# Performance work log

Measured on AMD Instinct MI355X. Metric: run time of the kernel, lower is better.

Reference implementation:

```python
import jax, jax.numpy as jnp
import numpy as np

B, T, IN, H, OUT = 1024, 512, 16, 64, 8


def setup_inputs() -> dict:
    key = jax.random.key(0)
    ks = jax.random.split(key, 7)
    s = 1.0 / np.sqrt(H)
    return {
        "x": jax.random.normal(ks[0], (B, T, IN), dtype=jnp.float32),
        "W_ih": jax.random.normal(ks[1], (4 * H, IN), dtype=jnp.float32) * s,
        "W_hh": jax.random.normal(ks[2], (4 * H, H), dtype=jnp.float32) * s,
        "b_ih": jax.random.normal(ks[3], (4 * H,), dtype=jnp.float32) * s,
        "b_hh": jax.random.normal(ks[4], (4 * H,), dtype=jnp.float32) * s,
        "W_fc": jax.random.normal(ks[5], (OUT, H), dtype=jnp.float32) * s,
        "b_fc": jax.random.normal(ks[6], (OUT,), dtype=jnp.float32) * s,
    }


def reference(x, W_ih, W_hh, b_ih, b_hh, W_fc, b_fc):
    Bq, Tq, _ = x.shape
    Hq = W_hh.shape[1]
    # Precompute input contribution for all timesteps: [T, B, 4H]
    xw = jnp.einsum("bti,gi->tbg", x, W_ih) + b_ih + b_hh

    def step(carry, xw_t):
        h, c = carry
        gates = xw_t + h @ W_hh.T  # [B, 4H]
        i, f, g, o = jnp.split(gates, 4, axis=-1)  # PyTorch gate order i,f,g,o
        i = jax.nn.sigmoid(i)
        f = jax.nn.sigmoid(f)
        g = jnp.tanh(g)
        o = jax.nn.sigmoid(o)
        c = f * c + i * g
        h = o * jnp.tanh(c)
        return (h, c), None

    h0 = jnp.zeros((Bq, Hq), dtype=x.dtype)
    c0 = jnp.zeros((Bq, Hq), dtype=x.dtype)
    (h_last, _), _ = jax.lax.scan(step, (h0, c0), xw)

    # fc on last timestep only, then sigmoid -> [B, 1, OUT]
    out = jax.nn.sigmoid(h_last @ W_fc.T + b_fc)
    return out[:, None, :]
```

## Files before the change

### kernel.cpp

```cpp
#include <hip/hip_runtime.h>
#include <math.h>


#define LSTM_T 512
#define LSTM_IN 16
#define LSTM_H 64
#define LSTM_OUT 8
#define BT 2
#define HSTRIDE 136

#define L2E   1.44269504088896340736f
#define L2E2  2.88539008177792681472f

typedef _Float16 half8  __attribute__((ext_vector_type(8)));
typedef float    floatx4 __attribute__((ext_vector_type(4)));

static __device__ __forceinline__ float fast_rcp(float x) { return __builtin_amdgcn_rcpf(x); }
static __device__ __forceinline__ float fast_exp2(float x) { return __builtin_amdgcn_exp2f(x); }
static __device__ __forceinline__ float sigm2(float p) { return fast_rcp(1.0f + fast_exp2(-p)); }
static __device__ __forceinline__ void pin4(int4& v) {
    asm volatile("" : "+v"(v.x), "+v"(v.y), "+v"(v.z), "+v"(v.w));
}
static __device__ __forceinline__ void pinf4(float4& v) {
    asm volatile("" : "+v"(v.x), "+v"(v.y), "+v"(v.z), "+v"(v.w));
}
static __device__ __forceinline__ void lite_barrier() {
    asm volatile("s_waitcnt lgkmcnt(0)\n\ts_barrier" ::: "memory");
}
static __device__ __forceinline__ unsigned pk2h(float a, float b) {
    return __builtin_bit_cast(unsigned, __builtin_amdgcn_cvt_pkrtz(a, b));
}
static __device__ __forceinline__ half8 to_h8(float4 a, float4 b) {
    uint4 u = make_uint4(pk2h(a.x, a.y), pk2h(a.z, a.w), pk2h(b.x, b.y), pk2h(b.z, b.w));
    return __builtin_bit_cast(half8, u);
}
static __device__ __forceinline__ int4 cvt8h(float4 a, float4 b) {
    return __builtin_bit_cast(int4, to_h8(a, b));
}
static __device__ __forceinline__ float4 ld4(const float* p) {
    return *reinterpret_cast<const float4*>(p);
}
static __device__ __forceinline__ float4 scl4(float4 v, float s) {
    return make_float4(s * v.x, s * v.y, s * v.z, s * v.w);
}
static __device__ __forceinline__ float sel4(floatx4 v, bool r0, bool r1) {
    float lo = r0 ? v[1] : v[0];
    float hi = r0 ? v[3] : v[2];
    return r1 ? hi : lo;
}
static __device__ __forceinline__ float dpp8(float v) {
    int r = __builtin_amdgcn_update_dpp(0, __builtin_bit_cast(int, v),
                                        0x128, 0xF, 0xF, false);
    return __builtin_bit_cast(float, r);
}

__global__ __launch_bounds__(256, 2)
void lstm_mfma_kernel(const float* __restrict__ x,
                      const float* __restrict__ W_ih,
                      const float* __restrict__ W_hh,
                      const float* __restrict__ b_ih,
                      const float* __restrict__ b_hh,
                      const float* __restrict__ W_fc,
                      const float* __restrict__ b_fc,
                      float* __restrict__ out) {
    const int tid   = threadIdx.x;
    const int lane  = tid & 63;
    const int w     = tid >> 6;
    const int q     = lane >> 4;
    const int m     = lane & 15;
    const int b     = m & 1;
    const int rho   = (m >> 1) & 3;
    const bool r0   = (rho & 1) != 0;
    const bool r1   = (rho & 2) != 0;
    const bool h1   = (m & 8) != 0;
    const int jmine = 16 * w + 4 * q + rho;
    const bool wr   = (m < 8);
    const int woff  = b * HSTRIDE + jmine + (h1 ? 64 : 0);
    const int bbase = blockIdx.x * BT;

    const float a1 = h1 ? 1.0f : 0.0f;
    const float b1 = h1 ? -2.0f : 1.0f;

    __shared__ __align__(16) _Float16 hbuf[2][BT][HSTRIDE];
    __shared__ __align__(16) float hfin[BT][LSTM_H];

    int4 Ah[4][2], Ax[4];
    float4 bias4[4];
    #pragma unroll
    for (int tt = 0; tt < 4; ++tt) {
        const float sc = (tt == 2) ? L2E2 : -L2E;
        const int gt = tt * 64 + 16 * w + m;
        #pragma unroll
        for (int c = 0; c < 2; ++c) {
            const float* s = W_hh + gt * LSTM_H + 32 * c + 8 * q;
            Ah[tt][c] = cvt8h(scl4(ld4(s), sc), scl4(ld4(s + 4), sc));
            pin4(Ah[tt][c]);
        }
        float4 xa = make_float4(0.f, 0.f, 0.f, 0.f), xb = xa;
        if (q < 2) {
            const float* s = W_ih + gt * LSTM_IN + 8 * q;
            xa = ld4(s); xb = ld4(s + 4);
        }
        Ax[tt] = cvt8h(scl4(xa, sc), scl4(xb, sc));
        pin4(Ax[tt]);
        const int gb = tt * 64 + 16 * w + 4 * q;
        float4 bi = ld4(b_ih + gb), bh = ld4(b_hh + gb);
        bias4[tt] = make_float4(sc * (bi.x + bh.x), sc * (bi.y + bh.y),
                                sc * (bi.z + bh.z), sc * (bi.w + bh.w));
        pinf4(bias4[tt]);
    }

    if (tid < 64) {
        int bb = tid >> 5, jj = tid & 31;
        reinterpret_cast<int*>(&hbuf[0][bb][0])[jj] = 0;
    }

    const float* xp = x + (size_t)(bbase + b) * LSTM_T * LSTM_IN + 8 * q;
    float4 xA0 = make_float4(0.f, 0.f, 0.f, 0.f), xA1 = xA0;
    float4 xB0 = xA0, xB1 = xA0;
    if (q < 2) {
        xA0 = ld4(xp);              xA1 = ld4(xp + 4);
        xB0 = ld4(xp + LSTM_IN);    xB1 = ld4(xp + LSTM_IN + 4);
    }
    __syncthreads();

    float cs = 0.0f, hreg = 0.0f;

#define STEP(T_, X0, X1)                                                        \
    {                                                                           \
        const _Float16* cur = &hbuf[(T_) & 1][0][0];                            \
        _Float16*       nxt = &hbuf[((T_) + 1) & 1][0][0];                      \
         \
        half8 bh0 = *reinterpret_cast<const half8*>(cur + b * HSTRIDE + 8 * q); \
        half8 bh1 = *reinterpret_cast<const half8*>(cur + b * HSTRIDE + 32 + 8 * q); \
        half8 xf = to_h8(X0, X1);                                               \
        floatx4 acc[4];                                                         \
        _Pragma("unroll")                                                       \
        for (int tt = 0; tt < 4; ++tt)                                          \
            acc[tt] = __builtin_amdgcn_mfma_f32_16x16x32_f16(                   \
                __builtin_bit_cast(half8, Ax[tt]), xf,                          \
                __builtin_bit_cast(floatx4, bias4[tt]), 0, 0, 0);               \
                       \
        if (q < 2 && (T_) + 2 < LSTM_T) {                                       \
            X0 = ld4(xp + (size_t)((T_) + 2) * LSTM_IN);                        \
            X1 = ld4(xp + (size_t)((T_) + 2) * LSTM_IN + 4);                    \
        }                                                                       \
        _Pragma("unroll")                                                       \
        for (int tt = 0; tt < 4; ++tt)                                          \
            acc[tt] = __builtin_amdgcn_mfma_f32_16x16x32_f16(                   \
                __builtin_bit_cast(half8, Ah[tt][0]), bh0, acc[tt], 0, 0, 0);   \
        _Pragma("unroll")                                                       \
        for (int tt = 0; tt < 4; ++tt)                                          \
            acc[tt] = __builtin_amdgcn_mfma_f32_16x16x32_f16(                   \
                __builtin_bit_cast(half8, Ah[tt][1]), bh1, acc[tt], 0, 0, 0);   \
        __builtin_amdgcn_s_setprio(1);                                          \
               \
        floatx4 v1, v2;                                                         \
        _Pragma("unroll")                                                       \
        for (int r = 0; r < 4; ++r) {                                           \
            v1[r] = h1 ? acc[2][r] : acc[1][r];                                 \
            v2[r] = h1 ? acc[3][r] : acc[0][r];                                 \
        }                                                                       \
        float u1 = sel4(v1, r0, r1);                                            \
        float u2 = sel4(v2, r0, r1);                                            \
                  \
        float act1 = fmaf(b1, fast_rcp(1.0f + fast_exp2(u1)), a1);              \
        float act2 = fast_rcp(1.0f + fast_exp2(u2));          \
        float act2K = act2 * L2E2;                   \
            \
        float g_in = dpp8(act1);                                                \
        float o_in = dpp8(act2);                                                \
        \
        cs = fmaf(act1, cs, act2K * g_in);                                      \
        float th = fmaf(-2.0f, fast_rcp(1.0f + fast_exp2(cs)), 1.0f);           \
        hreg = o_in * th;                                                       \
                   \
        nxt[woff] = (_Float16)hreg;                                             \
        __builtin_amdgcn_s_setprio(0);                                          \
        lite_barrier();                                                         \
    }

    for (int t = 0; t < LSTM_T; t += 2) {
        STEP(t,     xA0, xA1)
        STEP(t + 1, xB0, xB1)
    }
#undef STEP

    if (wr) hfin[b][jmine] = hreg;
    __syncthreads();

    if (tid < BT * LSTM_OUT) {
        int bb = tid >> 3, o = tid & 7;
        float s = b_fc[o];
        #pragma unroll
        for (int j4 = 0; j4 < LSTM_H / 4; ++j4) {
            float4 wv = ld4(W_fc + o * LSTM_H + 4 * j4);
            float4 hv = *reinterpret_cast<const float4*>(&hfin[bb][4 * j4]);
            s = fmaf(wv.x, hv.x, s);
            s = fmaf(wv.y, hv.y, s);
            s = fmaf(wv.z, hv.z, s);
            s = fmaf(wv.w, hv.w, s);
        }
        out[(size_t)(bbase + bb) * LSTM_OUT + o] = sigm2(s * L2E);
    }
}

extern "C" void kernel_launch(void* const* d_in, const int* in_sizes, int n_in,
                              void* d_out, int out_size, void* d_ws, size_t ws_size,
                              hipStream_t stream) {
    const float* x    = (const float*)d_in[0];
    const float* W_ih = (const float*)d_in[1];
    const float* W_hh = (const float*)d_in[2];
    const float* b_ih = (const float*)d_in[3];
    const float* b_hh = (const float*)d_in[4];
    const float* W_fc = (const float*)d_in[5];
    const float* b_fc = (const float*)d_in[6];
    float* out = (float*)d_out;

    lstm_mfma_kernel<<<1024 / BT, 256, 0, stream>>>(
        x, W_ih, W_hh, b_ih, b_hh, W_fc, b_fc, out);
}
```

Before: 251.4 us.

## Process four batch rows per block and pipeline input MFMAs off the critical path

Each block now handles four batch rows instead of two, with every lane computing all four gates for its own (batch, hidden) element. This drops the split-gate layout and the DPP exchange. The input-projection MFMA for the next step is issued after the recurrent MFMAs, so only the two h-dependent MFMAs sit on the serial dependency chain. Occupancy is lowered to one block per SIMD set and the grid is halved, which trades fewer blocks and less latency hiding for fewer barriers per row and more useful lanes per MFMA.

```diff
diff --git a/kernel.cpp b/kernel.cpp
--- a/kernel.cpp
+++ b/kernel.cpp
@@ -6,8 +6,8 @@
 #define LSTM_IN 16
 #define LSTM_H 64
 #define LSTM_OUT 8
-#define BT 2
-#define HSTRIDE 136
+#define BT 4
+#define HSTRIDE 80
 
 #define L2E   1.44269504088896340736f
 #define L2E2  2.88539008177792681472f
@@ -48,13 +48,8 @@
     float hi = r0 ? v[3] : v[2];
     return r1 ? hi : lo;
 }
-static __device__ __forceinline__ float dpp8(float v) {
-    int r = __builtin_amdgcn_update_dpp(0, __builtin_bit_cast(int, v),
-                                        0x128, 0xF, 0xF, false);
-    return __builtin_bit_cast(float, r);
-}
-
-__global__ __launch_bounds__(256, 2)
+
+__global__ __launch_bounds__(256, 1)
 void lstm_mfma_kernel(const float* __restrict__ x,
                       const float* __restrict__ W_ih,
                       const float* __restrict__ W_hh,
@@ -68,21 +63,15 @@
     const int w     = tid >> 6;
     const int q     = lane >> 4;
     const int m     = lane & 15;
-    const int b     = m & 1;
-    const int rho   = (m >> 1) & 3;
-    const bool r0   = (rho & 1) != 0;
-    const bool r1   = (rho & 2) != 0;
-    const bool h1   = (m & 8) != 0;
-    const int jmine = 16 * w + 4 * q + rho;
-    const bool wr   = (m < 8);
-    const int woff  = b * HSTRIDE + jmine + (h1 ? 64 : 0);
+    const int b     = m & 3;
+    const int r     = m >> 2;
+    const bool r0   = (r & 1) != 0;
+    const bool r1   = (r & 2) != 0;
+    const int jmine = 16 * w + 4 * q + r;
     const int bbase = blockIdx.x * BT;
 
-    const float a1 = h1 ? 1.0f : 0.0f;
-    const float b1 = h1 ? -2.0f : 1.0f;
-
-    __shared__ __align__(16) _Float16 hbuf[2][BT][HSTRIDE];
-    __shared__ __align__(16) float hfin[BT][LSTM_H];
+    __shared__ __align__(128) _Float16 hbuf[2][BT][HSTRIDE];
+    __shared__ __align__(16)  float    hfin[BT][LSTM_H];
 
     int4 Ah[4][2], Ax[4];
     float4 bias4[4];
@@ -110,7 +99,7 @@
         pinf4(bias4[tt]);
     }
 
-    if (tid < 64) {
+    if (tid < 128) {
         int bb = tid >> 5, jj = tid & 31;
         reinterpret_cast<int*>(&hbuf[0][bb][0])[jj] = 0;
     }
@@ -122,6 +111,20 @@
         xA0 = ld4(xp);              xA1 = ld4(xp + 4);
         xB0 = ld4(xp + LSTM_IN);    xB1 = ld4(xp + LSTM_IN + 4);
     }
+
+    floatx4 accX[4];
+    {
+        half8 xf = to_h8(xA0, xA1);
+        #pragma unroll
+        for (int tt = 0; tt < 4; ++tt)
+            accX[tt] = __builtin_amdgcn_mfma_f32_16x16x32_f16(
+                __builtin_bit_cast(half8, Ax[tt]), xf,
+                __builtin_bit_cast(floatx4, bias4[tt]), 0, 0, 0);
+    }
+    if (q < 2) {
+        xA0 = ld4(xp + 2 * LSTM_IN);
+        xA1 = ld4(xp + 2 * LSTM_IN + 4);
+    }
     __syncthreads();
 
     float cs = 0.0f, hreg = 0.0f;
@@ -130,63 +133,57 @@
     {                                                                           \
         const _Float16* cur = &hbuf[(T_) & 1][0][0];                            \
         _Float16*       nxt = &hbuf[((T_) + 1) & 1][0][0];                      \
-         \
+               \
         half8 bh0 = *reinterpret_cast<const half8*>(cur + b * HSTRIDE + 8 * q); \
         half8 bh1 = *reinterpret_cast<const half8*>(cur + b * HSTRIDE + 32 + 8 * q); \
-        half8 xf = to_h8(X0, X1);                                               \
         floatx4 acc[4];                                                         \
         _Pragma("unroll")                                                       \
         for (int tt = 0; tt < 4; ++tt)                                          \
             acc[tt] = __builtin_amdgcn_mfma_f32_16x16x32_f16(                   \
-                __builtin_bit_cast(half8, Ax[tt]), xf,                          \
-                __builtin_bit_cast(floatx4, bias4[tt]), 0, 0, 0);               \
-                       \
-        if (q < 2 && (T_) + 2 < LSTM_T) {                                       \
-            X0 = ld4(xp + (size_t)((T_) + 2) * LSTM_IN);                        \
-            X1 = ld4(xp + (size_t)((T_) + 2) * LSTM_IN + 4);                    \
-        }                                                                       \
-        _Pragma("unroll")                                                       \
-        for (int tt = 0; tt < 4; ++tt)                                          \
-            acc[tt] = __builtin_amdgcn_mfma_f32_16x16x32_f16(                   \
-                __builtin_bit_cast(half8, Ah[tt][0]), bh0, acc[tt], 0, 0, 0);   \
+                __builtin_bit_cast(half8, Ah[tt][0]), bh0, accX[tt], 0, 0, 0);  \
         _Pragma("unroll")                                                       \
         for (int tt = 0; tt < 4; ++tt)                                          \
             acc[tt] = __builtin_amdgcn_mfma_f32_16x16x32_f16(                   \
                 __builtin_bit_cast(half8, Ah[tt][1]), bh1, acc[tt], 0, 0, 0);   \
-        __builtin_amdgcn_s_setprio(1);                                          \
-               \
-        floatx4 v1, v2;                                                         \
-        _Pragma("unroll")                                                       \
-        for (int r = 0; r < 4; ++r) {                                           \
-            v1[r] = h1 ? acc[2][r] : acc[1][r];                                 \
-            v2[r] = h1 ? acc[3][r] : acc[0][r];                                 \
+           \
+          \
+        if ((T_) + 1 < LSTM_T) {                                                \
+            half8 xf = to_h8(X0, X1);                                           \
+            _Pragma("unroll")                                                   \
+            for (int tt = 0; tt < 4; ++tt)                                      \
+                accX[tt] = __builtin_amdgcn_mfma_f32_16x16x32_f16(              \
+                    __builtin_bit_cast(half8, Ax[tt]), xf,                      \
+                    __builtin_bit_cast(floatx4, bias4[tt]), 0, 0, 0);           \
         }                                                                       \
-        float u1 = sel4(v1, r0, r1);                                            \
-        float u2 = sel4(v2, r0, r1);                                            \
-                  \
-        float act1 = fmaf(b1, fast_rcp(1.0f + fast_exp2(u1)), a1);              \
-        float act2 = fast_rcp(1.0f + fast_exp2(u2));          \
-        float act2K = act2 * L2E2;                   \
-            \
-        float g_in = dpp8(act1);                                                \
-        float o_in = dpp8(act2);                                                \
-        \
-        cs = fmaf(act1, cs, act2K * g_in);                                      \
+                                        \
+        if (q < 2 && (T_) + 3 < LSTM_T) {                                       \
+            X0 = ld4(xp + (size_t)((T_) + 3) * LSTM_IN);                        \
+            X1 = ld4(xp + (size_t)((T_) + 3) * LSTM_IN + 4);                    \
+        }                                                                       \
+                               \
+        float ui = sel4(acc[0], r0, r1);                                        \
+        float uf = sel4(acc[1], r0, r1);                                        \
+        float ug = sel4(acc[2], r0, r1);                                        \
+        float uo = sel4(acc[3], r0, r1);                                        \
+        float ff = fast_rcp(1.0f + fast_exp2(uf));                              \
+        float ii = fast_rcp(1.0f + fast_exp2(ui));                              \
+        float gg = fmaf(-2.0f, fast_rcp(1.0f + fast_exp2(ug)), 1.0f);           \
+        float oo = fast_rcp(1.0f + fast_exp2(uo));                              \
+        cs = fmaf(ff, cs, (L2E2 * ii) * gg);                                    \
         float th = fmaf(-2.0f, fast_rcp(1.0f + fast_exp2(cs)), 1.0f);           \
-        hreg = o_in * th;                                                       \
-                   \
-        nxt[woff] = (_Float16)hreg;                                             \
-        __builtin_amdgcn_s_setprio(0);                                          \
+        hreg = oo * th;                                                         \
+                     \
+        nxt[b * HSTRIDE + jmine] = (_Float16)hreg;                              \
         lite_barrier();                                                         \
     }
 
     for (int t = 0; t < LSTM_T; t += 2) {
-        STEP(t,     xA0, xA1)
-        STEP(t + 1, xB0, xB1)
+        STEP(t,     xB0, xB1)
+        STEP(t + 1, xA0, xA1)
     }
 #undef STEP
 
-    if (wr) hfin[b][jmine] = hreg;
+    hfin[b][jmine] = hreg;
     __syncthreads();
 
     if (tid < BT * LSTM_OUT) {
```

New measurement: 269.4 us. 7.2% more time.

## Split recurrent MFMA chains and interleave gate activations with remaining matmuls

Applied to the files above, without the earlier changes.

The per-step recurrent MFMA accumulation is split into two independent half-K chains (bh0 half seeded with the input projection, bh1 half seeded with zero) that are summed afterwards, which shortens the dependent MFMA chain on the serial critical path. The f/g gates are computed first, and their exp is issued while the i/o MFMAs are still running, so transcendental work overlaps the matrix pipeline. Both lane halves now compute the cell state redundantly and write h, which removes the write predicate and shrinks the LDS row stride. The cost is extra VALU adds and selects, plus duplicated activation work per lane.

```diff
diff --git a/kernel.cpp b/kernel.cpp
--- a/kernel.cpp
+++ b/kernel.cpp
@@ -7,7 +7,7 @@
 #define LSTM_H 64
 #define LSTM_OUT 8
 #define BT 2
-#define HSTRIDE 136
+#define HSTRIDE 80
 
 #define L2E   1.44269504088896340736f
 #define L2E2  2.88539008177792681472f
@@ -74,15 +74,13 @@
     const bool r1   = (rho & 2) != 0;
     const bool h1   = (m & 8) != 0;
     const int jmine = 16 * w + 4 * q + rho;
-    const bool wr   = (m < 8);
-    const int woff  = b * HSTRIDE + jmine + (h1 ? 64 : 0);
     const int bbase = blockIdx.x * BT;
 
     const float a1 = h1 ? 1.0f : 0.0f;
     const float b1 = h1 ? -2.0f : 1.0f;
 
-    __shared__ __align__(16) _Float16 hbuf[2][BT][HSTRIDE];
-    __shared__ __align__(16) float hfin[BT][LSTM_H];
+    __shared__ __align__(128) _Float16 hbuf[2][BT][HSTRIDE];
+    __shared__ __align__(16)  float    hfin[BT][LSTM_H];
 
     int4 Ah[4][2], Ax[4];
     float4 bias4[4];
@@ -110,9 +108,12 @@
         pinf4(bias4[tt]);
     }
 
-    if (tid < 64) {
-        int bb = tid >> 5, jj = tid & 31;
-        reinterpret_cast<int*>(&hbuf[0][bb][0])[jj] = 0;
+    float4 zc4 = make_float4(0.f, 0.f, 0.f, 0.f);
+    pinf4(zc4);
+    const floatx4 zc = __builtin_bit_cast(floatx4, zc4);
+
+    if (tid < 80) {
+        reinterpret_cast<int*>(&hbuf[0][0][0])[tid] = 0;
     }
 
     const float* xp = x + (size_t)(bbase + b) * LSTM_T * LSTM_IN + 8 * q;
@@ -130,52 +131,69 @@
     {                                                                           \
         const _Float16* cur = &hbuf[(T_) & 1][0][0];                            \
         _Float16*       nxt = &hbuf[((T_) + 1) & 1][0][0];                      \
-         \
+                                               \
         half8 bh0 = *reinterpret_cast<const half8*>(cur + b * HSTRIDE + 8 * q); \
         half8 bh1 = *reinterpret_cast<const half8*>(cur + b * HSTRIDE + 32 + 8 * q); \
+            \
         half8 xf = to_h8(X0, X1);                                               \
-        floatx4 acc[4];                                                         \
-        _Pragma("unroll")                                                       \
-        for (int tt = 0; tt < 4; ++tt)                                          \
-            acc[tt] = __builtin_amdgcn_mfma_f32_16x16x32_f16(                   \
-                __builtin_bit_cast(half8, Ax[tt]), xf,                          \
-                __builtin_bit_cast(floatx4, bias4[tt]), 0, 0, 0);               \
-                       \
+        floatx4 aXi = __builtin_amdgcn_mfma_f32_16x16x32_f16(                   \
+            __builtin_bit_cast(half8, Ax[0]), xf,                               \
+            __builtin_bit_cast(floatx4, bias4[0]), 0, 0, 0);                    \
+        floatx4 aXf = __builtin_amdgcn_mfma_f32_16x16x32_f16(                   \
+            __builtin_bit_cast(half8, Ax[1]), xf,                               \
+            __builtin_bit_cast(floatx4, bias4[1]), 0, 0, 0);                    \
+        floatx4 aXg = __builtin_amdgcn_mfma_f32_16x16x32_f16(                   \
+            __builtin_bit_cast(half8, Ax[2]), xf,                               \
+            __builtin_bit_cast(floatx4, bias4[2]), 0, 0, 0);                    \
+        floatx4 aXo = __builtin_amdgcn_mfma_f32_16x16x32_f16(                   \
+            __builtin_bit_cast(half8, Ax[3]), xf,                               \
+            __builtin_bit_cast(floatx4, bias4[3]), 0, 0, 0);                    \
+                    \
         if (q < 2 && (T_) + 2 < LSTM_T) {                                       \
             X0 = ld4(xp + (size_t)((T_) + 2) * LSTM_IN);                        \
             X1 = ld4(xp + (size_t)((T_) + 2) * LSTM_IN + 4);                    \
         }                                                                       \
-        _Pragma("unroll")                                                       \
-        for (int tt = 0; tt < 4; ++tt)                                          \
-            acc[tt] = __builtin_amdgcn_mfma_f32_16x16x32_f16(                   \
-                __builtin_bit_cast(half8, Ah[tt][0]), bh0, acc[tt], 0, 0, 0);   \
-        _Pragma("unroll")                                                       \
-        for (int tt = 0; tt < 4; ++tt)                                          \
-            acc[tt] = __builtin_amdgcn_mfma_f32_16x16x32_f16(                   \
-                __builtin_bit_cast(half8, Ah[tt][1]), bh1, acc[tt], 0, 0, 0);   \
+               \
+        floatx4 afA = __builtin_amdgcn_mfma_f32_16x16x32_f16(                   \
+            __builtin_bit_cast(half8, Ah[1][0]), bh0, aXf, 0, 0, 0);            \
+        floatx4 agA = __builtin_amdgcn_mfma_f32_16x16x32_f16(                   \
+            __builtin_bit_cast(half8, Ah[2][0]), bh0, aXg, 0, 0, 0);            \
+        floatx4 afB = __builtin_amdgcn_mfma_f32_16x16x32_f16(                   \
+            __builtin_bit_cast(half8, Ah[1][1]), bh1, zc, 0, 0, 0);             \
+        floatx4 agB = __builtin_amdgcn_mfma_f32_16x16x32_f16(                   \
+            __builtin_bit_cast(half8, Ah[2][1]), bh1, zc, 0, 0, 0);             \
         __builtin_amdgcn_s_setprio(1);                                          \
-               \
-        floatx4 v1, v2;                                                         \
-        _Pragma("unroll")                                                       \
-        for (int r = 0; r < 4; ++r) {                                           \
-            v1[r] = h1 ? acc[2][r] : acc[1][r];                                 \
-            v2[r] = h1 ? acc[3][r] : acc[0][r];                                 \
-        }                                                                       \
-        float u1 = sel4(v1, r0, r1);                                            \
-        float u2 = sel4(v2, r0, r1);                                            \
-                  \
-        float act1 = fmaf(b1, fast_rcp(1.0f + fast_exp2(u1)), a1);              \
-        float act2 = fast_rcp(1.0f + fast_exp2(u2));          \
-        float act2K = act2 * L2E2;                   \
-            \
+        float uf = sel4(afA, r0, r1) + sel4(afB, r0, r1);                       \
+        float ug = sel4(agA, r0, r1) + sel4(agB, r0, r1);                       \
+        float u1 = h1 ? ug : uf;                                                \
+        float e1 = fast_exp2(u1);                                               \
+                                        \
+        floatx4 aiA = __builtin_amdgcn_mfma_f32_16x16x32_f16(                   \
+            __builtin_bit_cast(half8, Ah[0][0]), bh0, aXi, 0, 0, 0);            \
+        floatx4 aoA = __builtin_amdgcn_mfma_f32_16x16x32_f16(                   \
+            __builtin_bit_cast(half8, Ah[3][0]), bh0, aXo, 0, 0, 0);            \
+        floatx4 aiB = __builtin_amdgcn_mfma_f32_16x16x32_f16(                   \
+            __builtin_bit_cast(half8, Ah[0][1]), bh1, zc, 0, 0, 0);             \
+        floatx4 aoB = __builtin_amdgcn_mfma_f32_16x16x32_f16(                   \
+            __builtin_bit_cast(half8, Ah[3][1]), bh1, zc, 0, 0, 0);             \
+        float act1 = fmaf(b1, fast_rcp(1.0f + e1), a1);                         \
+        float ui = sel4(aiA, r0, r1) + sel4(aiB, r0, r1);                       \
+        float uo = sel4(aoA, r0, r1) + sel4(aoB, r0, r1);                       \
+        float u2 = h1 ? uo : ui;                                                \
+        float act2 = fast_rcp(1.0f + fast_exp2(u2));                            \
+                                              \
         float g_in = dpp8(act1);                                                \
         float o_in = dpp8(act2);                                                \
-        \
-        cs = fmaf(act1, cs, act2K * g_in);                                      \
+                 \
+        float fsel = h1 ? g_in : act1;                            \
+        float isel = h1 ? o_in : act2;                            \
+        float gsel = h1 ? act1 : g_in;                            \
+        float osel = h1 ? act2 : o_in;                            \
+        cs = fmaf(fsel, cs, (L2E2 * isel) * gsel);                              \
         float th = fmaf(-2.0f, fast_rcp(1.0f + fast_exp2(cs)), 1.0f);           \
-        hreg = o_in * th;                                                       \
-                   \
-        nxt[woff] = (_Float16)hreg;                                             \
+        hreg = osel * th;                                                       \
+             \
+        nxt[b * HSTRIDE + jmine] = (_Float16)hreg;                              \
         __builtin_amdgcn_s_setprio(0);                                          \
         lite_barrier();                                                         \
     }
@@ -186,7 +204,7 @@
     }
 #undef STEP
 
-    if (wr) hfin[b][jmine] = hreg;
+    hfin[b][jmine] = hreg;
     __syncthreads();
 
     if (tid < BT * LSTM_OUT) {
```

Result: slower. 284.2 us (+13.1%).
